# Performance work log

Hardware: AMD Instinct MI355X
Metric: run time of the kernel (lower is better)

## Reference

```python
import jax, jax.numpy as jnp
import numpy as np

B, N, D, H = 1, 1024, 512, 16
DH = D // H
NBINS = 68
R0 = 10.0
K_ITER = 20
LAM = 1.0


def _ln(x, w, b):
    m = x.mean(-1, keepdims=True)
    v = ((x - m) ** 2).mean(-1, keepdims=True)
    return (x - m) * jax.lax.rsqrt(v + 1e-5) * w + b


def _ln_plain(x):
    m = x.mean(-1, keepdims=True)
    v = ((x - m) ** 2).mean(-1, keepdims=True)
    return (x - m) * jax.lax.rsqrt(v + 1e-5)


def setup_inputs():
    key = jax.random.key(0)
    k = jax.random.split(key, 16)
    s = 0.02
    return {
        "h": jax.random.normal(k[0], (B, N, D), jnp.float32),
        "x_res": jax.random.normal(k[1], (B, N, 3), jnp.float32) * 3.0,
        "mu": jax.random.uniform(k[2], (B, H, N), jnp.float32, 0.5, 1.5) / N,
        "nu": jax.random.uniform(k[3], (B, H, N), jnp.float32, 0.5, 1.5) / N,
        "log_u_prev": jnp.zeros((B, H, N), jnp.float32),
        "log_v_prev": jnp.zeros((B, H, N), jnp.float32),
        "mask": jnp.ones((B, N), jnp.float32),
        "ln_attn_w": jnp.ones((D,), jnp.float32),
        "ln_attn_b": jnp.zeros((D,), jnp.float32),
        "wq": jax.random.normal(k[4], (D, D), jnp.float32) * s,
        "wk": jax.random.normal(k[5], (D, D), jnp.float32) * s,
        "wv": jax.random.normal(k[6], (D, D), jnp.float32) * s,
        "wg": jax.random.normal(k[7], (D, D), jnp.float32) * s,
        "wo": jax.random.normal(k[8], (D, D), jnp.float32) * s,
        "gamma": jax.random.normal(k[9], (H,), jnp.float32) * 1e-4,
        "pos_weight": jax.random.normal(k[10], (NBINS, H), jnp.float32) * s,
        "w_dist_logit": jnp.full((H,), -2.0, jnp.float32),
        "ln_ff_w": jnp.ones((D,), jnp.float32),
        "ln_ff_b": jnp.zeros((D,), jnp.float32),
        "sw_w1": jax.random.normal(k[11], (4 * D, D), jnp.float32) * s,
        "sw_w3": jax.random.normal(k[12], (4 * D, D), jnp.float32) * s,
        "sw_w2": jax.random.normal(k[13], (D, 4 * D), jnp.float32) * s,
        "pos_bins": jax.random.randint(k[14], (B, N, N), 0, NBINS, jnp.int32),
        "eps": jnp.array([0.5] * 4 + [1.0] * 4 + [2.0] * 4 + [4.0] * 4, jnp.float32),
    }


def reference(h, x_res, mu, nu, log_u_prev, log_v_prev, mask, ln_attn_w, ln_attn_b,
              wq, wk, wv, wg, wo, gamma, pos_weight, w_dist_logit,
              ln_ff_w, ln_ff_b, sw_w1, sw_w3, sw_w2, pos_bins, eps):
    h_n = _ln(h, ln_attn_w, ln_attn_b)

    def heads(w):
        return (h_n @ w.T).reshape(B, N, H, DH).transpose(0, 2, 1, 3)  # (B,H,N,DH)

    Q = _ln_plain(heads(wq))
    K = _ln_plain(heads(wk))
    V = heads(wv)
    G = heads(wg)

    # similarity + position bias + distance-gated kernel
    S = jnp.einsum('bhid,bhjd->bhij', Q, K) / np.float32(np.sqrt(DH))  # (B,H,N,N)
    bias = pos_weight[pos_bins].transpose(0, 3, 1, 2)                 # (B,H,N,N)
    d2 = jnp.sum((x_res[:, :, None, :] - x_res[:, None, :, :]) ** 2, -1)  # (B,N,N)
    w_dist = jax.nn.sigmoid(w_dist_logit)                             # (H,)
    logits = S + bias - w_dist[None, :, None, None] * d2[:, None, :, :] / (R0 ** 2)

    pair_mask = mask[:, None, :, None] * mask[:, None, None, :]       # (B,1,N,N)
    logK = jnp.where(pair_mask > 0, logits / eps[None, :, None, None], -1e9)

    # unbalanced log-domain Sinkhorn, 20 iterations, warm-started
    fi = (LAM / (LAM + eps))[None, :, None]                           # (1,H,1)
    log_mu = jnp.log(jnp.clip(mu, 1e-8))
    log_nu = jnp.log(jnp.clip(nu, 1e-8))
    log_u, log_v = log_u_prev, log_v_prev
    lse = jax.scipy.special.logsumexp
    for _ in range(K_ITER):
        log_u = fi * (log_mu - lse(logK + log_v[:, :, None, :], axis=-1))
        log_v = fi * (log_nu - lse(logK + log_u[:, :, :, None], axis=-2))

    P = jnp.exp(logK + log_u[:, :, :, None] + log_v[:, :, None, :]) * pair_mask
    row = jnp.clip(P.sum(-1, keepdims=True), 1e-8)
    Pn = P / row                                                      # row-normalized plan

    attn = jnp.einsum('bhij,bhjd->bhid', Pn, V) * jax.nn.sigmoid(G)
    o = attn.transpose(0, 2, 1, 3).reshape(B, N, D)
    h = h + (o @ wo.T) * mask[:, :, None]

    # centroid EGNN coordinate update
    x_cent = jnp.einsum('bhij,bjc->bhic', Pn, x_res)                  # (B,H,N,3)
    delta = x_res[:, None, :, :] - x_cent
    x_upd = jnp.einsum('h,bhnc->bnc', jnp.tanh(gamma) / H, delta) * mask[:, :, None]
    x_res = x_res + x_upd

    # SwiGLU FFN
    h2 = _ln(h, ln_ff_w, ln_ff_b)
    ff = (jax.nn.silu(h2 @ sw_w1.T) * (h2 @ sw_w3.T)) @ sw_w2.T
    h = h + ff * mask[:, :, None]
    return h, x_res, log_u, log_v
```

## Files before the change

kernel.cpp:

```cpp
#include <hip/hip_runtime.h>
#include <cstddef>
#include <cstdint>

#define N_TOK 1024
#define D_MODEL 512
#define H_HEADS 16
#define DHEAD 32
#define DFF 2048

typedef __attribute__((ext_vector_type(8))) short short8;
typedef __attribute__((ext_vector_type(4))) float f32x4_t;

__device__ __forceinline__ float sigmoidf_(float x){ return 1.f/(1.f+__expf(-x)); }

__device__ __forceinline__ unsigned short f2bf(float f){
  union { float f; unsigned u; } v; v.f = f;
  unsigned r = (v.u + 0x7FFFu + ((v.u >> 16) & 1u)) >> 16;
  return (unsigned short)r;
}
__device__ __forceinline__ float bf_lo(unsigned u){ return __uint_as_float(u << 16); }
__device__ __forceinline__ float bf_hi(unsigned u){ return __uint_as_float(u & 0xFFFF0000u); }

__device__ __forceinline__ int swz_head(int b){ return (b & 7) + 8 * ((b >> 3) & 1); }

__global__ __launch_bounds__(256) void ln_rows(const float* __restrict__ x,
                                               const float* __restrict__ w,
                                               const float* __restrict__ b,
                                               unsigned short* __restrict__ y) {
  int row = blockIdx.x;
  const float* xr = x + (size_t)row * D_MODEL;
  float s = 0.f, s2 = 0.f;
  for (int i = threadIdx.x; i < D_MODEL; i += 256) { float v = xr[i]; s += v; s2 += v*v; }
  #pragma unroll
  for (int off = 32; off; off >>= 1) { s += __shfl_down(s, off); s2 += __shfl_down(s2, off); }
  __shared__ float rs[4], rs2[4];
  int wave = threadIdx.x >> 6, lane = threadIdx.x & 63;
  if (lane == 0) { rs[wave] = s; rs2[wave] = s2; }
  __syncthreads();
  s  = rs[0] + rs[1] + rs[2] + rs[3];
  s2 = rs2[0] + rs2[1] + rs2[2] + rs2[3];
  float mean = s * (1.f / D_MODEL);
  float var  = s2 * (1.f / D_MODEL) - mean * mean;
  float r = rsqrtf(var + 1e-5f);
  unsigned short* yr = y + (size_t)row * D_MODEL;
  for (int i = threadIdx.x; i < D_MODEL; i += 256)
    yr[i] = f2bf((xr[i] - mean) * r * w[i] + b[i]);
}

__global__ __launch_bounds__(256) void conv_weights(const float* __restrict__ wq,
                                                    const float* __restrict__ wk,
                                                    const float* __restrict__ wv,
                                                    const float* __restrict__ wg,
                                                    const float* __restrict__ wo,
                                                    const float* __restrict__ w1,
                                                    const float* __restrict__ w3,
                                                    const float* __restrict__ w2,
                                                    unsigned short* __restrict__ dst) {
  size_t i = ((size_t)blockIdx.x * 256 + threadIdx.x) * 4;
  const float* src; size_t off;
  if      (i < 262144)  { src = wq; off = i; }
  else if (i < 524288)  { src = wk; off = i - 262144; }
  else if (i < 786432)  { src = wv; off = i - 524288; }
  else if (i < 1048576) { src = wg; off = i - 786432; }
  else if (i < 1310720) { src = wo; off = i - 1048576; }
  else if (i < 2359296) { src = w1; off = i - 1310720; }
  else if (i < 3407872) { src = w3; off = i - 2359296; }
  else                  { src = w2; off = i - 3407872; }
  float4 v = *(const float4*)&src[off];
  unsigned lo = ((unsigned)f2bf(v.y) << 16) | f2bf(v.x);
  unsigned hi = ((unsigned)f2bf(v.w) << 16) | f2bf(v.z);
  *(uint2*)&dst[i] = make_uint2(lo, hi);
}

__global__ __launch_bounds__(256) void gemm_mfma(const unsigned short* __restrict__ A,
                                                 const unsigned short* __restrict__ B,
                                                 float* __restrict__ C,
                                                 int M, int K, int Nout,
                                                 const float* __restrict__ addmat,
                                                 const float* __restrict__ maskrow) {
  __shared__ unsigned short As[128][40];
  __shared__ unsigned short Bs[128][40];
  int t = threadIdx.x;
  int m0 = blockIdx.y * 128, n0 = blockIdx.x * 128;
  int wave = t >> 6, lane = t & 63;
  int wm = (wave >> 1) * 64, wn = (wave & 1) * 64;
  int lm = lane & 15, quad = lane >> 4;
  f32x4_t zero = {0.f, 0.f, 0.f, 0.f};
  f32x4_t acc[4][4];
  #pragma unroll
  for (int i = 0; i < 4; ++i)
    #pragma unroll
    for (int j = 0; j < 4; ++j) acc[i][j] = zero;

  int sr = t >> 2, sc = (t & 3) * 8;
  for (int kk = 0; kk < K; kk += 32) {
    #pragma unroll
    for (int c = 0; c < 2; ++c) {
      int r = sr + c * 64;
      *(uint4*)&As[r][sc] = *(const uint4*)&A[(size_t)(m0 + r) * K + kk + sc];
      *(uint4*)&Bs[r][sc] = *(const uint4*)&B[(size_t)(n0 + r) * K + kk + sc];
    }
    __syncthreads();
    short8 af[4], bfr[4];
    #pragma unroll
    for (int mt = 0; mt < 4; ++mt)
      af[mt] = *(const short8*)&As[wm + mt * 16 + lm][quad * 8];
    #pragma unroll
    for (int nt = 0; nt < 4; ++nt)
      bfr[nt] = *(const short8*)&Bs[wn + nt * 16 + lm][quad * 8];
    #pragma unroll
    for (int mt = 0; mt < 4; ++mt)
      #pragma unroll
      for (int nt = 0; nt < 4; ++nt)
        acc[mt][nt] = __builtin_amdgcn_mfma_f32_16x16x32_bf16(af[mt], bfr[nt], acc[mt][nt], 0, 0, 0);
    __syncthreads();
  }
  #pragma unroll
  for (int mt = 0; mt < 4; ++mt) {
    #pragma unroll
    for (int reg = 0; reg < 4; ++reg) {
      int gm = m0 + wm + mt * 16 + quad * 4 + reg;
      float mk = maskrow ? maskrow[gm] : 0.f;
      #pragma unroll
      for (int nt = 0; nt < 4; ++nt) {
        int gn = n0 + wn + nt * 16 + lm;
        float v = acc[mt][nt][reg];
        if (addmat) v = addmat[(size_t)gm * Nout + gn] + v * mk;
        C[(size_t)gm * Nout + gn] = v;
      }
    }
  }
}

__global__ __launch_bounds__(256) void gemm_mfma64(const unsigned short* __restrict__ A,
                                                   const unsigned short* __restrict__ B,
                                                   float* __restrict__ C,
                                                   int M, int K, int Nout,
                                                   const float* __restrict__ addmat,
                                                   const float* __restrict__ maskrow) {
  __shared__ unsigned short As[64][40];
  __shared__ unsigned short Bs[64][40];
  int t = threadIdx.x;
  int m0 = blockIdx.y * 64, n0 = blockIdx.x * 64;
  int wave = t >> 6, lane = t & 63;
  int wm = (wave >> 1) * 32, wn = (wave & 1) * 32;
  int lm = lane & 15, quad = lane >> 4;
  f32x4_t zero = {0.f, 0.f, 0.f, 0.f};
  f32x4_t acc[2][2];
  #pragma unroll
  for (int i = 0; i < 2; ++i)
    #pragma unroll
    for (int j = 0; j < 2; ++j) acc[i][j] = zero;

  int sr = t >> 2, sc = (t & 3) * 8;
  for (int kk = 0; kk < K; kk += 32) {
    *(uint4*)&As[sr][sc] = *(const uint4*)&A[(size_t)(m0 + sr) * K + kk + sc];
    *(uint4*)&Bs[sr][sc] = *(const uint4*)&B[(size_t)(n0 + sr) * K + kk + sc];
    __syncthreads();
    short8 af[2], bfr[2];
    #pragma unroll
    for (int mt = 0; mt < 2; ++mt)
      af[mt] = *(const short8*)&As[wm + mt * 16 + lm][quad * 8];
    #pragma unroll
    for (int nt = 0; nt < 2; ++nt)
      bfr[nt] = *(const short8*)&Bs[wn + nt * 16 + lm][quad * 8];
    #pragma unroll
    for (int mt = 0; mt < 2; ++mt)
      #pragma unroll
      for (int nt = 0; nt < 2; ++nt)
        acc[mt][nt] = __builtin_amdgcn_mfma_f32_16x16x32_bf16(af[mt], bfr[nt], acc[mt][nt], 0, 0, 0);
    __syncthreads();
  }
  #pragma unroll
  for (int mt = 0; mt < 2; ++mt) {
    #pragma unroll
    for (int reg = 0; reg < 4; ++reg) {
      int gm = m0 + wm + mt * 16 + quad * 4 + reg;
      float mk = maskrow ? maskrow[gm] : 0.f;
      #pragma unroll
      for (int nt = 0; nt < 2; ++nt) {
        int gn = n0 + wn + nt * 16 + lm;
        float v = acc[mt][nt][reg];
        if (addmat) v = addmat[(size_t)gm * Nout + gn] + v * mk;
        C[(size_t)gm * Nout + gn] = v;
      }
    }
  }
}

__global__ __launch_bounds__(256) void headln(float* __restrict__ base, int ld) {
  int g = blockIdx.x * 256 + threadIdx.x;
  int i = g & (N_TOK - 1), hh = g >> 10;
  float* p = base + (size_t)i * ld + hh * DHEAD;
  float s = 0.f, s2 = 0.f;
  #pragma unroll
  for (int k = 0; k < DHEAD; ++k) { float v = p[k]; s += v; s2 += v*v; }
  float m = s * (1.f / DHEAD);
  float var = s2 * (1.f / DHEAD) - m * m;
  float r = rsqrtf(var + 1e-5f);
  #pragma unroll
  for (int k = 0; k < DHEAD; ++k) p[k] = (p[k] - m) * r;
}

__global__ __launch_bounds__(256) void build_W_mfma(const float* __restrict__ Q0,
                                                    const float* __restrict__ K0,
                                                    int ld,
                                                    const float* __restrict__ xres,
                                                    const int* __restrict__ bins,
                                                    const float* __restrict__ posw,
                                                    const float* __restrict__ wdl,
                                                    const float* __restrict__ epsp,
                                                    const float* __restrict__ mask,
                                                    unsigned short* __restrict__ Wm) {
  int b = blockIdx.x;
  int h = swz_head(b);
  int tile = b >> 4;
  int i0 = (tile >> 4) * 64, j0 = (tile & 15) * 64;
  __shared__ unsigned short Qs[64][40];
  __shared__ unsigned short Ks[64][40];
  __shared__ unsigned char  binsU[64][68];
  __shared__ unsigned short tileB[64][68];
  __shared__ float xi0[64], xi1[64], xi2[64], xj0[64], xj1[64], xj2[64];
  __shared__ float mi_s[64], mj_s[64], poswS[68];
  int t = threadIdx.x;
  {
    int r = t >> 2, c8 = (t & 3) * 8;
    const float* qsrc = Q0 + (size_t)(i0 + r) * ld + h * DHEAD + c8;
    const float* ksrc = K0 + (size_t)(j0 + r) * ld + h * DHEAD + c8;
    float4 qa = *(const float4*)qsrc, qb = *(const float4*)(qsrc + 4);
    float4 ka = *(const float4*)ksrc, kb = *(const float4*)(ksrc + 4);
    unsigned short* qd = &Qs[r][c8];
    qd[0]=f2bf(qa.x); qd[1]=f2bf(qa.y); qd[2]=f2bf(qa.z); qd[3]=f2bf(qa.w);
    qd[4]=f2bf(qb.x); qd[5]=f2bf(qb.y); qd[6]=f2bf(qb.z); qd[7]=f2bf(qb.w);
    unsigned short* kd = &Ks[r][c8];
    kd[0]=f2bf(ka.x); kd[1]=f2bf(ka.y); kd[2]=f2bf(ka.z); kd[3]=f2bf(ka.w);
    kd[4]=f2bf(kb.x); kd[5]=f2bf(kb.y); kd[6]=f2bf(kb.z); kd[7]=f2bf(kb.w);
  }
  {
    int rb = t >> 2, cb = (t & 3) * 16;
    const int* bsrc = bins + (size_t)(i0 + rb) * N_TOK + j0 + cb;
    #pragma unroll
    for (int c = 0; c < 4; ++c) {
      int4 b4 = *(const int4*)(bsrc + c * 4);
      uchar4 u4 = make_uchar4((unsigned char)b4.x, (unsigned char)b4.y,
                              (unsigned char)b4.z, (unsigned char)b4.w);
      *(uchar4*)&binsU[rb][cb + c * 4] = u4;
    }
  }
  if (t < 64) {
    xi0[t] = xres[(i0 + t) * 3 + 0]; xi1[t] = xres[(i0 + t) * 3 + 1]; xi2[t] = xres[(i0 + t) * 3 + 2];
    xj0[t] = xres[(j0 + t) * 3 + 0]; xj1[t] = xres[(j0 + t) * 3 + 1]; xj2[t] = xres[(j0 + t) * 3 + 2];
    mi_s[t] = mask[i0 + t]; mj_s[t] = mask[j0 + t];
  }
  if (t >= 64 && t < 132) poswS[t - 64] = posw[(t - 64) * H_HEADS + h];
  __syncthreads();
  int wave = t >> 6, lane = t & 63;
  int lm = lane & 15, quad = lane >> 4;
  int wm = (wave >> 1) * 32, wn = (wave & 1) * 32;
  f32x4_t zero = {0.f, 0.f, 0.f, 0.f};
  f32x4_t acc[2][2] = {{zero, zero}, {zero, zero}};
  short8 af[2], bfr[2];
  #pragma unroll
  for (int mt = 0; mt < 2; ++mt) af[mt] = *(const short8*)&Qs[wm + mt * 16 + lm][quad * 8];
  #pragma unroll
  for (int nt = 0; nt < 2; ++nt) bfr[nt] = *(const short8*)&Ks[wn + nt * 16 + lm][quad * 8];
  #pragma unroll
  for (int mt = 0; mt < 2; ++mt)
    #pragma unroll
    for (int nt = 0; nt < 2; ++nt)
      acc[mt][nt] = __builtin_amdgcn_mfma_f32_16x16x32_bf16(af[mt], bfr[nt], acc[mt][nt], 0, 0, 0);
  float wd = sigmoidf_(wdl[h]);
  float inv_eps = 1.f / epsp[h];
  const float inv_sqrt = 0.17677669529663687f;
  #pragma unroll
  for (int mt = 0; mt < 2; ++mt) {
    #pragma unroll
    for (int nt = 0; nt < 2; ++nt) {
      int col = wn + nt * 16 + lm;
      float xj0v = xj0[col], xj1v = xj1[col], xj2v = xj2[col], mj = mj_s[col];
      #pragma unroll
      for (int reg = 0; reg < 4; ++reg) {
        int row = wm + mt * 16 + quad * 4 + reg;
        float d0 = xi0[row] - xj0v, d1 = xi1[row] - xj1v, d2c = xi2[row] - xj2v;
        float d2 = d0*d0 + d1*d1 + d2c*d2c;
        float bias = poswS[binsU[row][col]];
        float logit = acc[mt][nt][reg] * inv_sqrt + bias - wd * d2 * 0.01f;
        float outv = (mi_s[row] * mj > 0.f) ? __expf(logit * inv_eps) : 0.f;
        tileB[row][col] = f2bf(outv);
      }
    }
  }
  __syncthreads();
  {
    int r = t >> 2, cb = (t & 3) * 16;
    unsigned short* dst = Wm + ((size_t)h * N_TOK + (i0 + r)) * N_TOK + j0 + cb;
    uint4 w0 = *(uint4*)&tileB[r][cb];
    uint4 w1v = *(uint4*)&tileB[r][cb + 8];
    *(uint4*)dst = w0;
    *(uint4*)(dst + 8) = w1v;
  }
}

__global__ __launch_bounds__(256) void build_vxt(const float* __restrict__ QKVG_,
                                                 const float* __restrict__ xres,
                                                 unsigned short* __restrict__ Vxt) {
  int h = blockIdx.x, j0 = blockIdx.y * 64;
  __shared__ float T[48][72];
  int t = threadIdx.x;
  {
    int j = t >> 2, c8 = (t & 3) * 8;
    const float* src = QKVG_ + (size_t)(j0 + j) * 2048 + 1024 + h * DHEAD + c8;
    float4 a = *(const float4*)src, b = *(const float4*)(src + 4);
    T[c8 + 0][j] = a.x; T[c8 + 1][j] = a.y; T[c8 + 2][j] = a.z; T[c8 + 3][j] = a.w;
    T[c8 + 4][j] = b.x; T[c8 + 5][j] = b.y; T[c8 + 6][j] = b.z; T[c8 + 7][j] = b.w;
  }
  if (t < 64) {
    int j = t;
    T[32][j] = xres[(j0 + j) * 3 + 0];
    T[33][j] = xres[(j0 + j) * 3 + 1];
    T[34][j] = xres[(j0 + j) * 3 + 2];
    T[35][j] = 1.f;
    #pragma unroll
    for (int d = 36; d < 48; ++d) T[d][j] = 0.f;
  }
  __syncthreads();
  for (int task = t; task < 384; task += 256) {
    int d = task >> 3, jc = (task & 7) * 8;
    float* s = &T[d][jc];
    unsigned a0 = ((unsigned)f2bf(s[1]) << 16) | f2bf(s[0]);
    unsigned a1 = ((unsigned)f2bf(s[3]) << 16) | f2bf(s[2]);
    unsigned a2 = ((unsigned)f2bf(s[5]) << 16) | f2bf(s[4]);
    unsigned a3 = ((unsigned)f2bf(s[7]) << 16) | f2bf(s[6]);
    *(uint4*)(Vxt + ((size_t)h * 48 + d) * N_TOK + j0 + jc) = make_uint4(a0, a1, a2, a3);
  }
}

__global__ __launch_bounds__(256) void sink_init(const float* __restrict__ mu,
                                                 const float* __restrict__ nu,
                                                 const float* __restrict__ lv0,
                                                 float* __restrict__ lmu,
                                                 float* __restrict__ lnu,
                                                 float* __restrict__ vtilde) {
  int i = blockIdx.x * 256 + threadIdx.x;
  lmu[i] = __logf(fmaxf(mu[i], 1e-8f));
  lnu[i] = __logf(fmaxf(nu[i], 1e-8f));
  vtilde[i] = __expf(lv0[i]);
}

__global__ __launch_bounds__(256) void sink_row(const unsigned short* __restrict__ Wm,
                                                const float* __restrict__ vtilde,
                                                const float* __restrict__ lmu,
                                                float* __restrict__ outlog,
                                                float* __restrict__ outexp,
                                                const float* __restrict__ epsp) {
  int b = blockIdx.x;
  int h = swz_head(b);
  int grp = b >> 4;
  int t = threadIdx.x;
  int wave = t >> 6, lane = t & 63;
  int sub = lane >> 4, l16 = lane & 15;
  int i = grp * 16 + wave * 4 + sub;
  const uint4* p = (const uint4*)(Wm + ((size_t)h * N_TOK + i) * N_TOK);
  const float4* vt = (const float4*)(vtilde + h * N_TOK);
  float s8[8];
  #pragma unroll
  for (int c = 0; c < 8; ++c) s8[c] = 0.f;
  #pragma unroll
  for (int it = 0; it < 8; ++it) {
    int j0 = it * 128 + l16 * 8;
    uint4 u = p[j0 >> 3];
    float4 va = vt[j0 >> 2];
    float4 vb = vt[(j0 >> 2) + 1];
    s8[0] += bf_lo(u.x) * va.x; s8[1] += bf_hi(u.x) * va.y;
    s8[2] += bf_lo(u.y) * va.z; s8[3] += bf_hi(u.y) * va.w;
    s8[4] += bf_lo(u.z) * vb.x; s8[5] += bf_hi(u.z) * vb.y;
    s8[6] += bf_lo(u.w) * vb.z; s8[7] += bf_hi(u.w) * vb.w;
  }
  float s = ((s8[0] + s8[1]) + (s8[2] + s8[3])) + ((s8[4] + s8[5]) + (s8[6] + s8[7]));
  #pragma unroll
  for (int off = 1; off <= 8; off <<= 1) s += __shfl_xor(s, off);
  if (l16 == 0) {
    float fi = 1.f / (1.f + epsp[h]);
    float val = fi * (lmu[h * N_TOK + i] - __logf(fmaxf(s, 1e-35f)));
    outlog[h * N_TOK + i] = val;
    outexp[h * N_TOK + i] = __expf(val);
  }
}

__global__ __launch_bounds__(256) void sink_row2(const unsigned short* __restrict__ Wm,
                                                 const float* __restrict__ part,
                                                 const float* __restrict__ lnu,
                                                 const float* __restrict__ lmu,
                                                 float* __restrict__ outlog,
                                                 float* __restrict__ outexp,
                                                 const float* __restrict__ epsp) {
  __shared__ float vt_lds[N_TOK];
  int b = blockIdx.x;
  int h = swz_head(b);
  int grp = b >> 4;
  int t = threadIdx.x;
  float fi = 1.f / (1.f + epsp[h]);
  {
    int j = t * 4;
    float4 p0 = *(const float4*)(part + 0 * 16384 + h * N_TOK + j);
    float4 p1 = *(const float4*)(part + 1 * 16384 + h * N_TOK + j);
    float4 p2 = *(const float4*)(part + 2 * 16384 + h * N_TOK + j);
    float4 p3 = *(const float4*)(part + 3 * 16384 + h * N_TOK + j);
    float4 ln4 = *(const float4*)(lnu + h * N_TOK + j);
    float s0 = (p0.x + p1.x) + (p2.x + p3.x);
    float s1 = (p0.y + p1.y) + (p2.y + p3.y);
    float s2 = (p0.z + p1.z) + (p2.z + p3.z);
    float s3 = (p0.w + p1.w) + (p2.w + p3.w);
    vt_lds[j + 0] = __expf(fi * (ln4.x - __logf(fmaxf(s0, 1e-35f))));
    vt_lds[j + 1] = __expf(fi * (ln4.y - __logf(fmaxf(s1, 1e-35f))));
    vt_lds[j + 2] = __expf(fi * (ln4.z - __logf(fmaxf(s2, 1e-35f))));
    vt_lds[j + 3] = __expf(fi * (ln4.w - __logf(fmaxf(s3, 1e-35f))));
  }
  __syncthreads();
  int wave = t >> 6, lane = t & 63;
  int sub = lane >> 4, l16 = lane & 15;
  int i = grp * 16 + wave * 4 + sub;
  const uint4* p = (const uint4*)(Wm + ((size_t)h * N_TOK + i) * N_TOK);
  float s8[8];
  #pragma unroll
  for (int c = 0; c < 8; ++c) s8[c] = 0.f;
  #pragma unroll
  for (int it = 0; it < 8; ++it) {
    int j0 = it * 128 + l16 * 8;
    uint4 u = p[j0 >> 3];
    float4 va = *(const float4*)&vt_lds[j0];
    float4 vb = *(const float4*)&vt_lds[j0 + 4];
    s8[0] += bf_lo(u.x) * va.x; s8[1] += bf_hi(u.x) * va.y;
    s8[2] += bf_lo(u.y) * va.z; s8[3] += bf_hi(u.y) * va.w;
    s8[4] += bf_lo(u.z) * vb.x; s8[5] += bf_hi(u.z) * vb.y;
    s8[6] += bf_lo(u.w) * vb.z; s8[7] += bf_hi(u.w) * vb.w;
  }
  float s = ((s8[0] + s8[1]) + (s8[2] + s8[3])) + ((s8[4] + s8[5]) + (s8[6] + s8[7]));
  #pragma unroll
  for (int off = 1; off <= 8; off <<= 1) s += __shfl_xor(s, off);
  if (l16 == 0) {
    float val = fi * (lmu[h * N_TOK + i] - __logf(fmaxf(s, 1e-35f)));
    outlog[h * N_TOK + i] = val;
    outexp[h * N_TOK + i] = __expf(val);
  }
}

__global__ __launch_bounds__(256) void sink_colp(const unsigned short* __restrict__ Wm,
                                                 const float* __restrict__ utilde,
                                                 float* __restrict__ part) {
  int b = blockIdx.x;
  int h = swz_head(b);
  int c = (b >> 4) & 3;
  int jt = (b >> 6) & 15;
  int j0 = jt * 64;
  int t = threadIdx.x;
  int jl = (t & 15) * 4;
  int ig = t >> 4;
  int r0 = c * 256 + ig * 16;
  const unsigned short* base = Wm + ((size_t)h * N_TOK + r0) * N_TOK + j0 + jl;
  const float* ut = utilde + h * N_TOK + r0;
  float a0 = 0.f, a1 = 0.f, a2 = 0.f, a3 = 0.f;
  #pragma unroll
  for (int r = 0; r < 16; ++r) {
    uint2 w = *(const uint2*)(base + (size_t)r * N_TOK);
    float u = ut[r];
    a0 += bf_lo(w.x) * u; a1 += bf_hi(w.x) * u;
    a2 += bf_lo(w.y) * u; a3 += bf_hi(w.y) * u;
  }
  __shared__ float red[16][68];
  red[ig][jl + 0] = a0; red[ig][jl + 1] = a1;
  red[ig][jl + 2] = a2; red[ig][jl + 3] = a3;
  __syncthreads();
  if (t < 64) {
    float s = 0.f;
    #pragma unroll
    for (int g = 0; g < 16; ++g) s += red[g][t];
    part[c * 16384 + h * N_TOK + j0 + t] = s;
  }
}

__global__ __launch_bounds__(256) void sink_fin(const float* __restrict__ part,
                                                const float* __restrict__ lnu,
                                                float* __restrict__ out_lv,
                                                float* __restrict__ vtilde,
                                                const float* __restrict__ epsp) {
  int h = blockIdx.x;
  int t = threadIdx.x;
  float fi = 1.f / (1.f + epsp[h]);
  int j = t * 4;
  float4 p0 = *(const float4*)(part + 0 * 16384 + h * N_TOK + j);
  float4 p1 = *(const float4*)(part + 1 * 16384 + h * N_TOK + j);
  float4 p2 = *(const float4*)(part + 2 * 16384 + h * N_TOK + j);
  float4 p3 = *(const float4*)(part + 3 * 16384 + h * N_TOK + j);
  float4 ln4 = *(const float4*)(lnu + h * N_TOK + j);
  float sv[4];
  sv[0] = (p0.x + p1.x) + (p2.x + p3.x);
  sv[1] = (p0.y + p1.y) + (p2.y + p3.y);
  sv[2] = (p0.z + p1.z) + (p2.z + p3.z);
  sv[3] = (p0.w + p1.w) + (p2.w + p3.w);
  float ln_[4] = {ln4.x, ln4.y, ln4.z, ln4.w};
  #pragma unroll
  for (int k = 0; k < 4; ++k) {
    float val = fi * (ln_[k] - __logf(fmaxf(sv[k], 1e-35f)));
    out_lv[h * N_TOK + j + k] = val;
    vtilde[h * N_TOK + j + k] = __expf(val);
  }
}

__global__ __launch_bounds__(256) void finalize_mfma(const unsigned short* __restrict__ Wm,
                                                     const float* __restrict__ vtilde,
                                                     const unsigned short* __restrict__ Vxt,
                                                     const float* __restrict__ G0, int ld,
                                                     const float* __restrict__ xres,
                                                     const float* __restrict__ mask,
                                                     unsigned short* __restrict__ o,
                                                     float* __restrict__ x_out,
                                                     const float* __restrict__ gamma) {
  int b = blockIdx.x;
  int h = swz_head(b);
  int mt = b >> 4;
  int t = threadIdx.x, wave = t >> 6, lane = t & 63;
  int lm = lane & 15, quad = lane >> 4;
  __shared__ float vts[N_TOK];
  ((float4*)vts)[t] = ((const float4*)(vtilde + h * N_TOK))[t];
  __syncthreads();
  int arow = mt * 64 + wave * 16 + lm;
  const unsigned short* Kr = Wm + ((size_t)h * N_TOK + arow) * N_TOK + quad * 8;
  const unsigned short* Bb = Vxt + (size_t)h * 48 * N_TOK + quad * 8;
  f32x4_t zero = {0.f, 0.f, 0.f, 0.f};
  f32x4_t acc[3] = {zero, zero, zero};
  for (int kk = 0; kk < N_TOK; kk += 32) {
    uint4 u = *(const uint4*)(Kr + kk);
    float4 la = *(const float4*)&vts[kk + quad * 8];
    float4 lb = *(const float4*)&vts[kk + quad * 8 + 4];
    float p0 = bf_lo(u.x) * la.x;
    float p1 = bf_hi(u.x) * la.y;
    float p2 = bf_lo(u.y) * la.z;
    float p3 = bf_hi(u.y) * la.w;
    float p4 = bf_lo(u.z) * lb.x;
    float p5 = bf_hi(u.z) * lb.y;
    float p6 = bf_lo(u.w) * lb.z;
    float p7 = bf_hi(u.w) * lb.w;
    union { uint4 u4; short8 s8; } pk;
    pk.u4 = make_uint4(((unsigned)f2bf(p1) << 16) | f2bf(p0),
                       ((unsigned)f2bf(p3) << 16) | f2bf(p2),
                       ((unsigned)f2bf(p5) << 16) | f2bf(p4),
                       ((unsigned)f2bf(p7) << 16) | f2bf(p6));
    short8 af = pk.s8;
    #pragma unroll
    for (int nt = 0; nt < 3; ++nt) {
      short8 bfrag = *(const short8*)(Bb + (size_t)(nt * 16 + lm) * N_TOK + kk);
      acc[nt] = __builtin_amdgcn_mfma_f32_16x16x32_bf16(af, bfrag, acc[nt], 0, 0, 0);
    }
  }
  float inv[4];
  #pragma unroll
  for (int reg = 0; reg < 4; ++reg) {
    float rsum = __shfl(acc[2][reg], (quad << 4) | 3, 64);
    inv[reg] = 1.f / fmaxf(rsum, 1e-30f);
  }
  #pragma unroll
  for (int nt = 0; nt < 2; ++nt) {
    int c = nt * 16 + lm;
    #pragma unroll
    for (int reg = 0; reg < 4; ++reg) {
      int r = mt * 64 + wave * 16 + quad * 4 + reg;
      float gv = G0[(size_t)r * ld + h * DHEAD + c];
      float ovl = acc[nt][reg] * inv[reg] * sigmoidf_(gv);
      o[(size_t)r * D_MODEL + h * DHEAD + c] = f2bf(ovl);
    }
  }
  if (lm < 3) {
    float tg = tanhf(gamma[h]) * (1.f / H_HEADS);
    #pragma unroll
    for (int reg = 0; reg < 4; ++reg) {
      int r = mt * 64 + wave * 16 + quad * 4 + reg;
      float xc = acc[2][reg] * inv[reg];
      float mi = mask[r];
      atomicAdd(&x_out[r * 3 + lm], tg * mi * (xres[r * 3 + lm] - xc));
    }
  }
}

__global__ __launch_bounds__(256) void silu_mul_bf(const float* __restrict__ ffab,
                                                   unsigned short* __restrict__ out, int n) {
  int i = blockIdx.x * 256 + threadIdx.x;
  if (i >= n) return;
  int row = i >> 11, col = i & 2047;
  float a = ffab[(size_t)row * 4096 + col];
  float bb = ffab[(size_t)row * 4096 + 2048 + col];
  out[i] = f2bf(a * sigmoidf_(a) * bb);
}

__global__ __launch_bounds__(256) void copyf(const float* __restrict__ src,
                                             float* __restrict__ dst, int n) {
  int i = blockIdx.x * 256 + threadIdx.x;
  if (i < n) dst[i] = src[i];
}

extern "C" void kernel_launch(void* const* d_in, const int* in_sizes, int n_in,
                              void* d_out, int out_size, void* d_ws, size_t ws_size,
                              hipStream_t stream) {
  const float* h_in  = (const float*)d_in[0];
  const float* x_res = (const float*)d_in[1];
  const float* mu    = (const float*)d_in[2];
  const float* nu    = (const float*)d_in[3];
  const float* lu0   = (const float*)d_in[4];
  const float* lv0   = (const float*)d_in[5];
  const float* mask  = (const float*)d_in[6];
  const float* lnw   = (const float*)d_in[7];
  const float* lnb   = (const float*)d_in[8];
  const float* wq    = (const float*)d_in[9];
  const float* wk    = (const float*)d_in[10];
  const float* wv    = (const float*)d_in[11];
  const float* wg    = (const float*)d_in[12];
  const float* wo    = (const float*)d_in[13];
  const float* gamma = (const float*)d_in[14];
  const float* posw  = (const float*)d_in[15];
  const float* wdl   = (const float*)d_in[16];
  const float* lnfw  = (const float*)d_in[17];
  const float* lnfb  = (const float*)d_in[18];
  const float* w1    = (const float*)d_in[19];
  const float* w3    = (const float*)d_in[20];
  const float* w2    = (const float*)d_in[21];
  const int*   bins  = (const int*)d_in[22];
  const float* eps   = (const float*)d_in[23];

  float* out    = (float*)d_out;
  float* out_h  = out;
  float* out_x  = out + 524288;
  float* out_lu = out + 527360;
  float* out_lv = out + 543744;

  float* ws = (float*)d_ws;
  float* QKVG  = ws;
  float* h_mid = ws + 2097152;
  unsigned short* U = (unsigned short*)(ws + 2621440);
  unsigned short* h_n_b  = U;
  unsigned short* h2_b   = U + 524288;
  unsigned short* o_b    = U + 1048576;
  unsigned short* wB     = U + 1572864;
  unsigned short* Wb   = (unsigned short*)(ws + 5636096);
  unsigned short* Vxt  = Wb + (size_t)H_HEADS * N_TOK * N_TOK;
  float* vtilde = (float*)(Vxt + 786432);
  float* utilde = vtilde + 16384;
  float* lmu    = utilde + 16384;
  float* lnu    = lmu + 16384;
  float* part   = lnu + 16384;
  unsigned short* ff_b = (unsigned short*)(part + 65536);
  float* ffab   = (float*)Wb;

  unsigned short* wQKVGb = wB;
  unsigned short* wob    = wB + 1048576;
  unsigned short* wFFb   = wB + 1310720;
  unsigned short* w2b    = wB + 3407872;

  dim3 b256(256);

  conv_weights<<<4352, b256, 0, stream>>>(wq, wk, wv, wg, wo, w1, w3, w2, wB);
  ln_rows<<<N_TOK, b256, 0, stream>>>(h_in, lnw, lnb, h_n_b);

  gemm_mfma<<<dim3(16, 8), b256, 0, stream>>>(h_n_b, wQKVGb, QKVG,
                                              N_TOK, D_MODEL, 2048, nullptr, nullptr);

  headln<<<128, b256, 0, stream>>>(QKVG, 2048);

  copyf<<<12, b256, 0, stream>>>(x_res, out_x, N_TOK * 3);

  build_W_mfma<<<4096, b256, 0, stream>>>(
      QKVG, QKVG + 512, 2048, x_res, bins, posw, wdl, eps, mask, Wb);
  build_vxt<<<dim3(H_HEADS, N_TOK / 64), b256, 0, stream>>>(QKVG, x_res, Vxt);

  sink_init<<<64, b256, 0, stream>>>(mu, nu, lv0, lmu, lnu, vtilde);

  sink_row<<<1024, b256, 0, stream>>>(Wb, vtilde, lmu, out_lu, utilde, eps);
  sink_colp<<<1024, b256, 0, stream>>>(Wb, utilde, part);
  for (int it = 1; it < 20; ++it) {
    sink_row2<<<1024, b256, 0, stream>>>(Wb, part, lnu, lmu, out_lu, utilde, eps);
    sink_colp<<<1024, b256, 0, stream>>>(Wb, utilde, part);
  }
  sink_fin<<<H_HEADS, b256, 0, stream>>>(part, lnu, out_lv, vtilde, eps);

  finalize_mfma<<<256, b256, 0, stream>>>(
      Wb, vtilde, Vxt, QKVG + 1536, 2048, x_res, mask, o_b, out_x, gamma);

  gemm_mfma64<<<dim3(8, 16), b256, 0, stream>>>(o_b, wob, h_mid,
                                                N_TOK, D_MODEL, D_MODEL, h_in, mask);

  ln_rows<<<N_TOK, b256, 0, stream>>>(h_mid, lnfw, lnfb, h2_b);

  gemm_mfma<<<dim3(32, 8), b256, 0, stream>>>(h2_b, wFFb, ffab,
                                              N_TOK, D_MODEL, 4096, nullptr, nullptr);
  silu_mul_bf<<<(N_TOK * DFF) / 256, b256, 0, stream>>>(ffab, ff_b, N_TOK * DFF);

  gemm_mfma64<<<dim3(8, 16), b256, 0, stream>>>(ff_b, w2b, out_h,
                                                N_TOK, DFF, D_MODEL, h_mid, mask);
}
```

Before: 424.9 us.

## Store Sinkhorn kernel matrix as per-row-scaled FP8 E4M3 instead of bf16

The bf16 exp-kernel matrix W is quantised to a software FP8 (E4M3-like) format with a per-row scale. The row max comes from atomicMax in build_W, and a new conv_w8 pass does the encoding. All Sinkhorn row/column passes and the finalize kernel read the 8-bit matrix and decode it in software, with the row scale folded into the row-update outputs. This halves the bytes streamed across the 40 memory-bound Sinkhorn passes. The cost is an extra encode pass, a bf16 temporary write/read, ALU work for decoding, and reduced precision in the transport plan.

Result: slower. 540.2 us (+27.1%).

```diff
diff --git a/kernel.cpp b/kernel.cpp
--- a/kernel.cpp
+++ b/kernel.cpp
@@ -20,6 +20,22 @@
 }
 __device__ __forceinline__ float bf_lo(unsigned u){ return __uint_as_float(u << 16); }
 __device__ __forceinline__ float bf_hi(unsigned u){ return __uint_as_float(u & 0xFFFF0000u); }
+
+__device__ __forceinline__ float dec8(unsigned x){
+  return (x >= 8u) ? __uint_as_float((x << 20) + 0x3C000000u)
+                   : (float)x * 0.001953125f;
+}
+__device__ __forceinline__ unsigned enc8(float f){
+  if (!(f > 0.f)) return 0u;
+  if (f >= 448.f) return 0x7Eu;
+  if (f >= 0.015625f) {
+    unsigned b = __float_as_uint(f);
+    unsigned r = b + 0x7FFFFu + ((b >> 20) & 1u);
+    return (r - 0x3C000000u) >> 20;
+  }
+  unsigned m = (unsigned)rintf(f * 512.f);
+  return m > 8u ? 8u : m;
+}
 
 __device__ __forceinline__ int swz_head(int b){ return (b & 7) + 8 * ((b >> 3) & 1); }
 
@@ -55,8 +71,11 @@
                                                     const float* __restrict__ w1,
                                                     const float* __restrict__ w3,
                                                     const float* __restrict__ w2,
-                                                    unsigned short* __restrict__ dst) {
-  size_t i = ((size_t)blockIdx.x * 256 + threadIdx.x) * 4;
+                                                    unsigned short* __restrict__ dst,
+                                                    unsigned* __restrict__ rowmaxU) {
+  size_t gid = (size_t)blockIdx.x * 256 + threadIdx.x;
+  if (gid < 16384) rowmaxU[gid] = 0u;
+  size_t i = gid * 4;
   const float* src; size_t off;
   if      (i < 262144)  { src = wq; off = i; }
   else if (i < 524288)  { src = wk; off = i - 262144; }
@@ -211,7 +230,8 @@
                                                     const float* __restrict__ wdl,
                                                     const float* __restrict__ epsp,
                                                     const float* __restrict__ mask,
-                                                    unsigned short* __restrict__ Wm) {
+                                                    unsigned short* __restrict__ Wtmp,
+                                                    unsigned* __restrict__ rowmaxU) {
   int b = blockIdx.x;
   int h = swz_head(b);
   int tile = b >> 4;
@@ -293,12 +313,57 @@
   __syncthreads();
   {
     int r = t >> 2, cb = (t & 3) * 16;
-    unsigned short* dst = Wm + ((size_t)h * N_TOK + (i0 + r)) * N_TOK + j0 + cb;
+    unsigned short* dst = Wtmp + ((size_t)h * N_TOK + (i0 + r)) * N_TOK + j0 + cb;
     uint4 w0 = *(uint4*)&tileB[r][cb];
     uint4 w1v = *(uint4*)&tileB[r][cb + 8];
     *(uint4*)dst = w0;
     *(uint4*)(dst + 8) = w1v;
   }
+  {
+    int r = t >> 2, cseg = (t & 3) * 16;
+    const unsigned* tp = (const unsigned*)&tileB[r][cseg];
+    float m = 0.f;
+    #pragma unroll
+    for (int k = 0; k < 8; ++k) {
+      unsigned w = tp[k];
+      m = fmaxf(m, fmaxf(bf_lo(w), bf_hi(w)));
+    }
+    m = fmaxf(m, __shfl_xor(m, 1));
+    m = fmaxf(m, __shfl_xor(m, 2));
+    if ((t & 3) == 0)
+      atomicMax(&rowmaxU[h * N_TOK + i0 + r], __float_as_uint(m));
+  }
+}
+
+__global__ __launch_bounds__(256) void conv_w8(const unsigned short* __restrict__ Wtmp,
+                                               const unsigned* __restrict__ rowmaxU,
+                                               unsigned char* __restrict__ W8,
+                                               float* __restrict__ rscale) {
+  int t = threadIdx.x;
+  int row = blockIdx.x * 4 + (t >> 6);
+  int lane = t & 63;
+  float rmax = fmaxf(__uint_as_float(rowmaxU[row]), 1e-30f);
+  float scale = rmax * (1.f / 448.f);
+  float inv = 448.f / rmax;
+  if (lane == 0) rscale[row] = scale;
+  const unsigned short* src = Wtmp + (size_t)row * N_TOK + lane * 16;
+  uint4 a = *(const uint4*)src;
+  uint4 bq = *(const uint4*)(src + 8);
+  unsigned e[16];
+  e[0] = enc8(bf_lo(a.x) * inv);  e[1] = enc8(bf_hi(a.x) * inv);
+  e[2] = enc8(bf_lo(a.y) * inv);  e[3] = enc8(bf_hi(a.y) * inv);
+  e[4] = enc8(bf_lo(a.z) * inv);  e[5] = enc8(bf_hi(a.z) * inv);
+  e[6] = enc8(bf_lo(a.w) * inv);  e[7] = enc8(bf_hi(a.w) * inv);
+  e[8] = enc8(bf_lo(bq.x) * inv); e[9] = enc8(bf_hi(bq.x) * inv);
+  e[10]= enc8(bf_lo(bq.y) * inv); e[11]= enc8(bf_hi(bq.y) * inv);
+  e[12]= enc8(bf_lo(bq.z) * inv); e[13]= enc8(bf_hi(bq.z) * inv);
+  e[14]= enc8(bf_lo(bq.w) * inv); e[15]= enc8(bf_hi(bq.w) * inv);
+  uint4 outw;
+  outw.x = e[0] | (e[1]<<8) | (e[2]<<16) | (e[3]<<24);
+  outw.y = e[4] | (e[5]<<8) | (e[6]<<16) | (e[7]<<24);
+  outw.z = e[8] | (e[9]<<8) | (e[10]<<16) | (e[11]<<24);
+  outw.w = e[12] | (e[13]<<8) | (e[14]<<16) | (e[15]<<24);
+  *(uint4*)(W8 + (size_t)row * N_TOK + lane * 16) = outw;
 }
 
 __global__ __launch_bounds__(256) void build_vxt(const float* __restrict__ QKVG_,
@@ -347,9 +412,36 @@
   vtilde[i] = __expf(lv0[i]);
 }
 
-__global__ __launch_bounds__(256) void sink_row(const unsigned short* __restrict__ Wm,
+__device__ __forceinline__ float row_dot8(const unsigned char* __restrict__ Wrow,
+                                          const float* __restrict__ vt, int l16) {
+  const uint4* p = (const uint4*)Wrow;
+  float s8[8];
+  #pragma unroll
+  for (int c = 0; c < 8; ++c) s8[c] = 0.f;
+  #pragma unroll
+  for (int q = 0; q < 4; ++q) {
+    int j0 = q * 256 + l16 * 16;
+    uint4 u = p[j0 >> 4];
+    float4 v0 = *(const float4*)&vt[j0];
+    float4 v1 = *(const float4*)&vt[j0 + 4];
+    float4 v2 = *(const float4*)&vt[j0 + 8];
+    float4 v3 = *(const float4*)&vt[j0 + 12];
+    s8[0] += dec8(u.x & 255u) * v0.x;         s8[1] += dec8((u.x >> 8) & 255u) * v0.y;
+    s8[2] += dec8((u.x >> 16) & 255u) * v0.z; s8[3] += dec8(u.x >> 24) * v0.w;
+    s8[4] += dec8(u.y & 255u) * v1.x;         s8[5] += dec8((u.y >> 8) & 255u) * v1.y;
+    s8[6] += dec8((u.y >> 16) & 255u) * v1.z; s8[7] += dec8(u.y >> 24) * v1.w;
+    s8[0] += dec8(u.z & 255u) * v2.x;         s8[1] += dec8((u.z >> 8) & 255u) * v2.y;
+    s8[2] += dec8((u.z >> 16) & 255u) * v2.z; s8[3] += dec8(u.z >> 24) * v2.w;
+    s8[4] += dec8(u.w & 255u) * v3.x;         s8[5] += dec8((u.w >> 8) & 255u) * v3.y;
+    s8[6] += dec8((u.w >> 16) & 255u) * v3.z; s8[7] += dec8(u.w >> 24) * v3.w;
+  }
+  return ((s8[0] + s8[1]) + (s8[2] + s8[3])) + ((s8[4] + s8[5]) + (s8[6] + s8[7]));
+}
+
+__global__ __launch_bounds__(256) void sink_row(const unsigned char* __restrict__ W8,
                                                 const float* __restrict__ vtilde,
                                                 const float* __restrict__ lmu,
+                                                const float* __restrict__ rscale,
                                                 float* __restrict__ outlog,
                                                 float* __restrict__ outexp,
                                                 const float* __restrict__ epsp) {
@@ -360,37 +452,23 @@
   int wave = t >> 6, lane = t & 63;
   int sub = lane >> 4, l16 = lane & 15;
   int i = grp * 16 + wave * 4 + sub;
-  const uint4* p = (const uint4*)(Wm + ((size_t)h * N_TOK + i) * N_TOK);
-  const float4* vt = (const float4*)(vtilde + h * N_TOK);
-  float s8[8];
-  #pragma unroll
-  for (int c = 0; c < 8; ++c) s8[c] = 0.f;
-  #pragma unroll
-  for (int it = 0; it < 8; ++it) {
-    int j0 = it * 128 + l16 * 8;
-    uint4 u = p[j0 >> 3];
-    float4 va = vt[j0 >> 2];
-    float4 vb = vt[(j0 >> 2) + 1];
-    s8[0] += bf_lo(u.x) * va.x; s8[1] += bf_hi(u.x) * va.y;
-    s8[2] += bf_lo(u.y) * va.z; s8[3] += bf_hi(u.y) * va.w;
-    s8[4] += bf_lo(u.z) * vb.x; s8[5] += bf_hi(u.z) * vb.y;
-    s8[6] += bf_lo(u.w) * vb.z; s8[7] += bf_hi(u.w) * vb.w;
-  }
-  float s = ((s8[0] + s8[1]) + (s8[2] + s8[3])) + ((s8[4] + s8[5]) + (s8[6] + s8[7]));
+  float s = row_dot8(W8 + ((size_t)h * N_TOK + i) * N_TOK, vtilde + h * N_TOK, l16);
   #pragma unroll
   for (int off = 1; off <= 8; off <<= 1) s += __shfl_xor(s, off);
   if (l16 == 0) {
+    float rs = rscale[h * N_TOK + i];
     float fi = 1.f / (1.f + epsp[h]);
-    float val = fi * (lmu[h * N_TOK + i] - __logf(fmaxf(s, 1e-35f)));
+    float val = fi * (lmu[h * N_TOK + i] - __logf(fmaxf(s * rs, 1e-35f)));
     outlog[h * N_TOK + i] = val;
-    outexp[h * N_TOK + i] = __expf(val);
-  }
-}
-
-__global__ __launch_bounds__(256) void sink_row2(const unsigned short* __restrict__ Wm,
+    outexp[h * N_TOK + i] = __expf(val) * rs;
+  }
+}
+
+__global__ __launch_bounds__(256) void sink_row2(const unsigned char* __restrict__ W8,
                                                  const float* __restrict__ part,
                                                  const float* __restrict__ lnu,
                                                  const float* __restrict__ lmu,
+                                                 const float* __restrict__ rscale,
                                                  float* __restrict__ outlog,
                                                  float* __restrict__ outexp,
                                                  const float* __restrict__ epsp) {
@@ -420,32 +498,18 @@
   int wave = t >> 6, lane = t & 63;
   int sub = lane >> 4, l16 = lane & 15;
   int i = grp * 16 + wave * 4 + sub;
-  const uint4* p = (const uint4*)(Wm + ((size_t)h * N_TOK + i) * N_TOK);
-  float s8[8];
-  #pragma unroll
-  for (int c = 0; c < 8; ++c) s8[c] = 0.f;
-  #pragma unroll
-  for (int it = 0; it < 8; ++it) {
-    int j0 = it * 128 + l16 * 8;
-    uint4 u = p[j0 >> 3];
-    float4 va = *(const float4*)&vt_lds[j0];
-    float4 vb = *(const float4*)&vt_lds[j0 + 4];
-    s8[0] += bf_lo(u.x) * va.x; s8[1] += bf_hi(u.x) * va.y;
-    s8[2] += bf_lo(u.y) * va.z; s8[3] += bf_hi(u.y) * va.w;
-    s8[4] += bf_lo(u.z) * vb.x; s8[5] += bf_hi(u.z) * vb.y;
-    s8[6] += bf_lo(u.w) * vb.z; s8[7] += bf_hi(u.w) * vb.w;
-  }
-  float s = ((s8[0] + s8[1]) + (s8[2] + s8[3])) + ((s8[4] + s8[5]) + (s8[6] + s8[7]));
+  float s = row_dot8(W8 + ((size_t)h * N_TOK + i) * N_TOK, vt_lds, l16);
   #pragma unroll
   for (int off = 1; off <= 8; off <<= 1) s += __shfl_xor(s, off);
   if (l16 == 0) {
-    float val = fi * (lmu[h * N_TOK + i] - __logf(fmaxf(s, 1e-35f)));
+    float rs = rscale[h * N_TOK + i];
+    float val = fi * (lmu[h * N_TOK + i] - __logf(fmaxf(s * rs, 1e-35f)));
     outlog[h * N_TOK + i] = val;
-    outexp[h * N_TOK + i] = __expf(val);
-  }
-}
-
-__global__ __launch_bounds__(256) void sink_colp(const unsigned short* __restrict__ Wm,
+    outexp[h * N_TOK + i] = __expf(val) * rs;
+  }
+}
+
+__global__ __launch_bounds__(256) void sink_colp(const unsigned char* __restrict__ W8,
                                                  const float* __restrict__ utilde,
                                                  float* __restrict__ part) {
   int b = blockIdx.x;
@@ -457,15 +521,15 @@
   int jl = (t & 15) * 4;
   int ig = t >> 4;
   int r0 = c * 256 + ig * 16;
-  const unsigned short* base = Wm + ((size_t)h * N_TOK + r0) * N_TOK + j0 + jl;
+  const unsigned char* base = W8 + ((size_t)h * N_TOK + r0) * N_TOK + j0 + jl;
   const float* ut = utilde + h * N_TOK + r0;
   float a0 = 0.f, a1 = 0.f, a2 = 0.f, a3 = 0.f;
   #pragma unroll
   for (int r = 0; r < 16; ++r) {
-    uint2 w = *(const uint2*)(base + (size_t)r * N_TOK);
+    unsigned w = *(const unsigned*)(base + (size_t)r * N_TOK);
     float u = ut[r];
-    a0 += bf_lo(w.x) * u; a1 += bf_hi(w.x) * u;
-    a2 += bf_lo(w.y) * u; a3 += bf_hi(w.y) * u;
+    a0 += dec8(w & 255u) * u;          a1 += dec8((w >> 8) & 255u) * u;
+    a2 += dec8((w >> 16) & 255u) * u;  a3 += dec8(w >> 24) * u;
   }
   __shared__ float red[16][68];
   red[ig][jl + 0] = a0; red[ig][jl + 1] = a1;
@@ -507,7 +571,7 @@
   }
 }
 
-__global__ __launch_bounds__(256) void finalize_mfma(const unsigned short* __restrict__ Wm,
+__global__ __launch_bounds__(256) void finalize_mfma(const unsigned char* __restrict__ W8,
                                                      const float* __restrict__ vtilde,
                                                      const unsigned short* __restrict__ Vxt,
                                                      const float* __restrict__ G0, int ld,
@@ -525,22 +589,22 @@
   ((float4*)vts)[t] = ((const float4*)(vtilde + h * N_TOK))[t];
   __syncthreads();
   int arow = mt * 64 + wave * 16 + lm;
-  const unsigned short* Kr = Wm + ((size_t)h * N_TOK + arow) * N_TOK + quad * 8;
+  const unsigned char* Kr = W8 + ((size_t)h * N_TOK + arow) * N_TOK + quad * 8;
   const unsigned short* Bb = Vxt + (size_t)h * 48 * N_TOK + quad * 8;
   f32x4_t zero = {0.f, 0.f, 0.f, 0.f};
   f32x4_t acc[3] = {zero, zero, zero};
   for (int kk = 0; kk < N_TOK; kk += 32) {
-    uint4 u = *(const uint4*)(Kr + kk);
+    uint2 u = *(const uint2*)(Kr + kk);
     float4 la = *(const float4*)&vts[kk + quad * 8];
     float4 lb = *(const float4*)&vts[kk + quad * 8 + 4];
-    float p0 = bf_lo(u.x) * la.x;
-    float p1 = bf_hi(u.x) * la.y;
-    float p2 = bf_lo(u.y) * la.z;
-    float p3 = bf_hi(u.y) * la.w;
-    float p4 = bf_lo(u.z) * lb.x;
-    float p5 = bf_hi(u.z) * lb.y;
-    float p6 = bf_lo(u.w) * lb.z;
-    float p7 = bf_hi(u.w) * lb.w;
+    float p0 = dec8(u.x & 255u) * la.x;
+    float p1 = dec8((u.x >> 8) & 255u) * la.y;
+    float p2 = dec8((u.x >> 16) & 255u) * la.z;
+    float p3 = dec8(u.x >> 24) * la.w;
+    float p4 = dec8(u.y & 255u) * lb.x;
+    float p5 = dec8((u.y >> 8) & 255u) * lb.y;
+    float p6 = dec8((u.y >> 16) & 255u) * lb.z;
+    float p7 = dec8(u.y >> 24) * lb.w;
     union { uint4 u4; short8 s8; } pk;
     pk.u4 = make_uint4(((unsigned)f2bf(p1) << 16) | f2bf(p0),
                        ((unsigned)f2bf(p3) << 16) | f2bf(p2),
@@ -640,15 +704,18 @@
   unsigned short* h2_b   = U + 524288;
   unsigned short* o_b    = U + 1048576;
   unsigned short* wB     = U + 1572864;
-  unsigned short* Wb   = (unsigned short*)(ws + 5636096);
-  unsigned short* Vxt  = Wb + (size_t)H_HEADS * N_TOK * N_TOK;
+  unsigned char*  W8   = (unsigned char*)(ws + 5636096);
+  unsigned short* Vxt  = (unsigned short*)(ws + 9830400);
   float* vtilde = (float*)(Vxt + 786432);
   float* utilde = vtilde + 16384;
   float* lmu    = utilde + 16384;
   float* lnu    = lmu + 16384;
-  float* part   = lnu + 16384;
+  float* rscale = lnu + 16384;
+  unsigned* rowmaxU = (unsigned*)(rscale + 16384);
+  float* part   = (float*)(rowmaxU + 16384);
   unsigned short* ff_b = (unsigned short*)(part + 65536);
-  float* ffab   = (float*)Wb;
+  unsigned short* Wtmp = (unsigned short*)(ff_b + 2097152);
+  float* ffab   = (float*)W8;
 
   unsigned short* wQKVGb = wB;
   unsigned short* wob    = wB + 1048576;
@@ -657,7 +724,7 @@
 
   dim3 b256(256);
 
-  conv_weights<<<4352, b256, 0, stream>>>(wq, wk, wv, wg, wo, w1, w3, w2, wB);
+  conv_weights<<<4352, b256, 0, stream>>>(wq, wk, wv, wg, wo, w1, w3, w2, wB, rowmaxU);
   ln_rows<<<N_TOK, b256, 0, stream>>>(h_in, lnw, lnb, h_n_b);
 
   gemm_mfma<<<dim3(16, 8), b256, 0, stream>>>(h_n_b, wQKVGb, QKVG,
@@ -668,21 +735,22 @@
   copyf<<<12, b256, 0, stream>>>(x_res, out_x, N_TOK * 3);
 
   build_W_mfma<<<4096, b256, 0, stream>>>(
-      QKVG, QKVG + 512, 2048, x_res, bins, posw, wdl, eps, mask, Wb);
+      QKVG, QKVG + 512, 2048, x_res, bins, posw, wdl, eps, mask, Wtmp, rowmaxU);
+  conv_w8<<<4096, b256, 0, stream>>>(Wtmp, rowmaxU, W8, rscale);
   build_vxt<<<dim3(H_HEADS, N_TOK / 64), b256, 0, stream>>>(QKVG, x_res, Vxt);
 
   sink_init<<<64, b256, 0, stream>>>(mu, nu, lv0, lmu, lnu, vtilde);
 
-  sink_row<<<1024, b256, 0, stream>>>(Wb, vtilde, lmu, out_lu, utilde, eps);
-  sink_colp<<<1024, b256, 0, stream>>>(Wb, utilde, part);
+  sink_row<<<1024, b256, 0, stream>>>(W8, vtilde, lmu, rscale, out_lu, utilde, eps);
+  sink_colp<<<1024, b256, 0, stream>>>(W8, utilde, part);
   for (int it = 1; it < 20; ++it) {
-    sink_row2<<<1024, b256, 0, stream>>>(Wb, part, lnu, lmu, out_lu, utilde, eps);
-    sink_colp<<<1024, b256, 0, stream>>>(Wb, utilde, part);
+    sink_row2<<<1024, b256, 0, stream>>>(W8, part, lnu, lmu, rscale, out_lu, utilde, eps);
+    sink_colp<<<1024, b256, 0, stream>>>(W8, utilde, part);
   }
   sink_fin<<<H_HEADS, b256, 0, stream>>>(part, lnu, out_lv, vtilde, eps);
 
   finalize_mfma<<<256, b256, 0, stream>>>(
-      Wb, vtilde, Vxt, QKVG + 1536, 2048, x_res, mask, o_b, out_x, gamma);
+      W8, vtilde, Vxt, QKVG + 1536, 2048, x_res, mask, o_b, out_x, gamma);
 
   gemm_mfma64<<<dim3(8, 16), b256, 0, stream>>>(o_b, wob, h_mid,
                                                 N_TOK, D_MODEL, D_MODEL, h_in, mask);
```
